# Kernel optimization log

Hardware: AMD Instinct MI355X
Metric: run time of the kernel (lower is better)

Reference implementation:

```python
import jax, jax.numpy as jnp
import numpy as np
from jax import lax

# hyperparameters (match init_kwargs)
N_INP, N_HID, N_OUT = 3, 64, 10
SEQ_LEN, N_ROLL, K = 8, 16, 3
DT, GAMMA, EPS = 0.042, 2.7, 4.7
H, W = 12, 10            # hard-coded in coRNNCell2's PixelwiseConv2d
PAD = (K - 1) // 2
BATCH = 16


def setup_inputs() -> dict:
    key = jax.random.key(0)
    ks = jax.random.split(key, 7)
    x = jax.random.normal(ks[0], (SEQ_LEN, BATCH, N_INP, H, W), dtype=jnp.float32)
    # readin: Conv2d(seq_len*n_inp -> 2*n_hid, k, padding=1, replicate)
    readin_w = jax.random.normal(ks[1], (2 * N_HID, SEQ_LEN * N_INP, K, K), dtype=jnp.float32) * 0.05
    readin_b = jax.random.normal(ks[2], (2 * N_HID,), dtype=jnp.float32) * 0.05
    # PixelwiseConv2d: per-output-pixel weights (out, in, k, k, H, W)
    pw_w = jax.random.normal(ks[3], (N_HID, 2 * N_HID, K, K, H, W), dtype=jnp.float32) * 0.05
    pw_b = jax.random.normal(ks[4], (N_HID, H, W), dtype=jnp.float32) * 0.05
    # readout: 1x1 conv (n_hid -> n_out)
    readout_w = jax.random.normal(ks[5], (N_OUT, N_HID), dtype=jnp.float32) * 0.05
    readout_b = jax.random.normal(ks[6], (N_OUT,), dtype=jnp.float32) * 0.05
    return {"x": x, "readin_w": readin_w, "readin_b": readin_b,
            "pw_w": pw_w, "pw_b": pw_b,
            "readout_w": readout_w, "readout_b": readout_b}


def _pixelwise_conv(x, pw_w, pw_b):
    # x: (B, 2*N_HID, H, W); zero padding like F.unfold(padding=PAD)
    B = x.shape[0]
    xp = jnp.pad(x, ((0, 0), (0, 0), (PAD, PAD), (PAD, PAD)))
    # patches ordered (c, i, j) to match unfold().view(B, C, k, k, H, W)
    patches = jnp.stack([xp[:, :, i:i + H, j:j + W]
                         for i in range(K) for j in range(K)], axis=2)
    patches = patches.reshape(B, 2 * N_HID, K, K, H, W)
    return jnp.einsum('bcijhw,ocijhw->bohw', patches, pw_w) + pw_b[None]


def reference(x, readin_w, readin_b, pw_w, pw_b, readout_w, readout_b):
    T, B = x.shape[0], x.shape[1]
    # 't b c h w -> b (t c) h w'
    xr = jnp.transpose(x, (1, 0, 2, 3, 4)).reshape(B, T * N_INP, H, W)
    # readin conv with replicate padding
    xr_p = jnp.pad(xr, ((0, 0), (0, 0), (PAD, PAD), (PAD, PAD)), mode='edge')
    h = lax.conv_general_dilated(xr_p, readin_w, (1, 1), 'VALID',
                                 dimension_numbers=('NCHW', 'OIHW', 'NCHW'))
    h = h + readin_b[None, :, None, None]
    hy, hz = h[:, :N_HID], h[:, N_HID:]

    def step(carry, _):
        hy, hz = carry
        pre = _pixelwise_conv(jnp.concatenate([hz, hy], axis=1), pw_w, pw_b)
        hz = hz + DT * (jnp.tanh(pre) - GAMMA * hy - EPS * hz)
        hy = hy + DT * hz
        return (hy, hz), None

    (hy, hz), _ = lax.scan(step, (hy, hz), None, length=N_ROLL)
    out = jnp.einsum('bchw,oc->bohw', hy, readout_w) + readout_b[None, :, None, None]
    return out
```

## Files before the change

### kernel.cpp

```cpp
#include <hip/hip_runtime.h>
#include <math.h>

#define N_INPC 3
#define N_HID 64
#define N_OUTC 10
#define SEQ_LEN 8
#define N_ROLL 16
#define DT 0.042f
#define GAMMA 2.7f
#define EPSC 4.7f
#define HH 12
#define WW 10
#define NPIX 120
#define BATCH 16
#define NC 128
#define NK 1152

typedef __attribute__((ext_vector_type(8))) short short8;
typedef __attribute__((ext_vector_type(4))) float f32x4;
typedef unsigned short ushort_t;

__device__ __forceinline__ ushort_t f2bf(float v) {
  union { float f; unsigned u; } x; x.f = v;
  unsigned r = x.u + 0x7fff + ((x.u >> 16) & 1);
  return (ushort_t)(r >> 16);
}

__global__ __launch_bounds__(256) void transpose2_kernel(
    const float* __restrict__ pw_w, ushort_t* __restrict__ Wt) {
  const int t = blockIdx.x * 256 + threadIdx.x;
  if (t >= 120 * 9216) return;
  const int p = t % 120;
  const int rest = t / 120;
  const int o = rest & 15;
  const int kg = (rest >> 4) & 3;
  const int ks = (rest >> 6) % 36;
  const int hot = (rest >> 6) / 36;
  const int o_g = (hot >> 1) * 32 + (hot & 1) * 16 + o;
  const int k0 = ks * 32 + kg * 8;
  ushort_t out8[8];
#pragma unroll
  for (int j = 0; j < 8; ++j) {
    const int kp = k0 + j;
    const int ij = kp >> 7;
    const int c = kp & 127;
    const float v = pw_w[((size_t)o_g * NK + c * 9 + ij) * NPIX + p];
    out8[j] = f2bf(v);
  }
  uint4 pack;
  pack.x = (unsigned)out8[0] | ((unsigned)out8[1] << 16);
  pack.y = (unsigned)out8[2] | ((unsigned)out8[3] << 16);
  pack.z = (unsigned)out8[4] | ((unsigned)out8[5] << 16);
  pack.w = (unsigned)out8[6] | ((unsigned)out8[7] << 16);
  *(uint4*)(Wt + ((size_t)p * 9216 + rest) * 8) = pack;
}

__global__ __launch_bounds__(256) void readin2_kernel(
    const float* __restrict__ x, const float* __restrict__ rw,
    const float* __restrict__ rb, float* __restrict__ Sm,
    ushort_t* __restrict__ Sg) {
  const int n = blockIdx.x * 256 + threadIdx.x;
  if (n >= BATCH * NC * NPIX) return;
  const int p = n % NPIX;
  const int oc = (n / NPIX) & 127;
  const int b = n / (NPIX * NC);
  const int ph = p / WW, pw_ = p % WW;
  float acc = rb[oc];
  for (int ch = 0; ch < SEQ_LEN * N_INPC; ++ch) {
    const int tt = ch / N_INPC, ic = ch % N_INPC;
    const float* xb = x + (((tt * BATCH + b) * N_INPC + ic) * HH) * WW;
    const float* wb = rw + (oc * (SEQ_LEN * N_INPC) + ch) * 9;
#pragma unroll
    for (int di = 0; di < 3; ++di) {
      int ih = ph + di - 1;
      ih = ih < 0 ? 0 : (ih > HH - 1 ? HH - 1 : ih);
#pragma unroll
      for (int dj = 0; dj < 3; ++dj) {
        int iw = pw_ + dj - 1;
        iw = iw < 0 ? 0 : (iw > WW - 1 ? WW - 1 : iw);
        acc += xb[ih * WW + iw] * wb[di * 3 + dj];
      }
    }
  }
  const int sc = (oc < 64) ? (64 + oc) : (oc - 64);
  const size_t idx = ((size_t)(p * BATCH + b)) * NC + sc;
  Sm[idx] = acc;
  Sg[idx] = f2bf(acc);
}

__global__ __launch_bounds__(256) void step2_kernel(
    const ushort_t* __restrict__ Wt, const ushort_t* __restrict__ Sg_cur,
    const float* __restrict__ Sm_cur, ushort_t* __restrict__ Sg_nxt,
    float* __restrict__ Sm_nxt, const float* __restrict__ pwb) {
  __shared__ short8 SA[2304];
  __shared__ f32x4 red[128];
  const int wg = blockIdx.x, p = wg >> 1, h = wg & 1;
  const int ph = p / WW, pw_ = p % WW;
  const int tid = threadIdx.x, wv = tid >> 6, l = tid & 63;

  {
    const int b = tid >> 4, m = tid & 15;
    const int bm = b * NC + m * 8;
#pragma unroll
    for (int q = 0; q < 9; ++q) {
      const int ih = ph + q / 3 - 1, iw = pw_ + q % 3 - 1;
      short8 v = {0, 0, 0, 0, 0, 0, 0, 0};
      if ((unsigned)ih < (unsigned)HH && (unsigned)iw < (unsigned)WW)
        v = *(const short8*)(Sg_cur + (size_t)(ih * WW + iw) * (BATCH * NC) + bm);
      const int row = q * 16 + m;
      SA[row * 16 + (b ^ m)] = v;
    }
  }
  __syncthreads();

  const int ot = wv & 1, kq = wv >> 1;
  const int kg = l >> 4, c16 = l & 15;
  const short8* __restrict__ WB =
      (const short8*)Wt + ((size_t)((p * 2 + h) * 2 + ot)) * 2304 + kg * 16 + c16;
  f32x4 acc0 = {0.f, 0.f, 0.f, 0.f}, acc1 = {0.f, 0.f, 0.f, 0.f};
#pragma unroll
  for (int ii = 0; ii < 9; ++ii) {
    const int ks0 = kq * 18 + ii * 2;
    {
      const int row = ks0 * 4 + kg;
      short8 av = SA[row * 16 + (c16 ^ (row & 15))];
      short8 bv = WB[ks0 * 64];
      acc0 = __builtin_amdgcn_mfma_f32_16x16x32_bf16(av, bv, acc0, 0, 0, 0);
    }
    {
      const int row = (ks0 + 1) * 4 + kg;
      short8 av = SA[row * 16 + (c16 ^ (row & 15))];
      short8 bv = WB[(ks0 + 1) * 64];
      acc1 = __builtin_amdgcn_mfma_f32_16x16x32_bf16(av, bv, acc1, 0, 0, 0);
    }
  }
  f32x4 acc = acc0 + acc1;

  if (wv >= 2) red[(wv - 2) * 64 + l] = acc;
  __syncthreads();
  if (wv < 2) {
    f32x4 part = red[wv * 64 + l];
    acc += part;
    const int o_g = h * 32 + ot * 16 + c16;
    const float pb = pwb[o_g * NPIX + p];
    const int b0 = (l >> 4) * 4;
#pragma unroll
    for (int r = 0; r < 4; ++r) {
      const int b = b0 + r;
      const size_t iz = ((size_t)(p * BATCH + b)) * NC + o_g;
      const float hz = Sm_cur[iz], hy = Sm_cur[iz + 64];
      const float pre = acc[r] + pb;
      const float hzn = hz + DT * (tanhf(pre) - GAMMA * hy - EPSC * hz);
      const float hyn = hy + DT * hzn;
      Sm_nxt[iz] = hzn;
      Sm_nxt[iz + 64] = hyn;
      Sg_nxt[iz] = f2bf(hzn);
      Sg_nxt[iz + 64] = f2bf(hyn);
    }
  }
}

__global__ __launch_bounds__(256) void readout2_kernel(
    const float* __restrict__ Sm, const float* __restrict__ row,
    const float* __restrict__ rob, float* __restrict__ out) {
  const int n = blockIdx.x * 256 + threadIdx.x;
  if (n >= BATCH * N_OUTC * NPIX) return;
  const int p = n % NPIX;
  const int o = (n / NPIX) % N_OUTC;
  const int b = n / (NPIX * N_OUTC);
  float acc = rob[o];
  const float* hy = Sm + ((size_t)(p * BATCH + b)) * NC + 64;
#pragma unroll 8
  for (int c = 0; c < 64; ++c) acc += hy[c] * row[o * 64 + c];
  out[n] = acc;
}

extern "C" void kernel_launch(void* const* d_in, const int* in_sizes, int n_in,
                              void* d_out, int out_size, void* d_ws, size_t ws_size,
                              hipStream_t stream) {
  const float* x         = (const float*)d_in[0];
  const float* readin_w  = (const float*)d_in[1];
  const float* readin_b  = (const float*)d_in[2];
  const float* pw_w      = (const float*)d_in[3];
  const float* pw_b      = (const float*)d_in[4];
  const float* readout_w = (const float*)d_in[5];
  const float* readout_b = (const float*)d_in[6];
  float* out = (float*)d_out;

  ushort_t* Wt  = (ushort_t*)d_ws;
  ushort_t* Sg0 = Wt + (size_t)120 * 9216 * 8;
  ushort_t* Sg1 = Sg0 + 245760;
  float*    Sm0 = (float*)(Sg1 + 245760);
  float*    Sm1 = Sm0 + 245760;

  transpose2_kernel<<<4320, 256, 0, stream>>>(pw_w, Wt);
  readin2_kernel<<<(BATCH * NC * NPIX + 255) / 256, 256, 0, stream>>>(
      x, readin_w, readin_b, Sm0, Sg0);

  ushort_t* gc = Sg0; float* mc = Sm0;
  ushort_t* gn = Sg1; float* mn = Sm1;
  for (int s = 0; s < N_ROLL; ++s) {
    step2_kernel<<<NPIX * 2, 256, 0, stream>>>(Wt, gc, mc, gn, mn, pw_b);
    ushort_t* tg = gc; gc = gn; gn = tg;
    float* tm = mc; mc = mn; mn = tm;
  }
  readout2_kernel<<<(BATCH * N_OUTC * NPIX + 255) / 256, 256, 0, stream>>>(
      mc, readout_w, readout_b, out);
}
```

Before: 212.4 us.

## Fuse recurrent steps into one persistent cooperative kernel with register-resident weights

Replaces the 16 per-step kernel launches with a single cooperative persistent kernel that loops over the time steps and uses grid.sync between them. Each workgroup keeps its bf16 weight slice in registers across all steps, and the fp32 hidden state stays in registers, so only bf16 state is exchanged through global memory. This removes launch gaps and repeated weight and state reloads. In exchange it adds the cost of grid-wide barriers, relies on all 240 blocks being co-resident, and raises register pressure.

Measured after the change: 652.4 us. 3.07x slower.

```diff
diff --git a/kernel.cpp b/kernel.cpp
--- a/kernel.cpp
+++ b/kernel.cpp
@@ -1,5 +1,8 @@
 #include <hip/hip_runtime.h>
+#include <hip/hip_cooperative_groups.h>
 #include <math.h>
+
+namespace cg = cooperative_groups;
 
 #define N_INPC 3
 #define N_HID 64
@@ -44,8 +47,7 @@
     const int kp = k0 + j;
     const int ij = kp >> 7;
     const int c = kp & 127;
-    const float v = pw_w[((size_t)o_g * NK + c * 9 + ij) * NPIX + p];
-    out8[j] = f2bf(v);
+    out8[j] = f2bf(pw_w[((size_t)o_g * NK + c * 9 + ij) * NPIX + p]);
   }
   uint4 pack;
   pack.x = (unsigned)out8[0] | ((unsigned)out8[1] << 16);
@@ -88,74 +90,102 @@
   Sg[idx] = f2bf(acc);
 }
 
-__global__ __launch_bounds__(256) void step2_kernel(
-    const ushort_t* __restrict__ Wt, const ushort_t* __restrict__ Sg_cur,
-    const float* __restrict__ Sm_cur, ushort_t* __restrict__ Sg_nxt,
-    float* __restrict__ Sm_nxt, const float* __restrict__ pwb) {
+__global__ __launch_bounds__(256, 1) void persist_kernel(
+    const ushort_t* __restrict__ Wt, ushort_t* __restrict__ SgA,
+    ushort_t* __restrict__ SgB, float* __restrict__ Sm,
+    const float* __restrict__ pwb) {
+  cg::grid_group grid = cg::this_grid();
   __shared__ short8 SA[2304];
   __shared__ f32x4 red[128];
   const int wg = blockIdx.x, p = wg >> 1, h = wg & 1;
   const int ph = p / WW, pw_ = p % WW;
   const int tid = threadIdx.x, wv = tid >> 6, l = tid & 63;
-
+  const int ot = wv & 1, kq = wv >> 1;
+  const int kg = l >> 4, c16 = l & 15;
+  const int o_g = h * 32 + ot * 16 + c16;
+
+  short8 breg[18];
   {
-    const int b = tid >> 4, m = tid & 15;
-    const int bm = b * NC + m * 8;
+    const short8* __restrict__ WB =
+        (const short8*)Wt + ((size_t)((p * 2 + h) * 2 + ot)) * 2304 + kg * 16 + c16;
+#pragma unroll
+    for (int j = 0; j < 18; ++j) breg[j] = WB[(size_t)(kq * 18 + j) * 64];
+  }
+  const float pb = pwb[o_g * NPIX + p];
+
+  const int b0 = (l >> 4) * 4;
+  float hzr[4], hyr[4];
+  if (wv < 2) {
+#pragma unroll
+    for (int r = 0; r < 4; ++r) {
+      const size_t iz = ((size_t)(p * BATCH + b0 + r)) * NC + o_g;
+      hzr[r] = Sm[iz];
+      hyr[r] = Sm[iz + 64];
+    }
+  }
+
+  const int ab = tid >> 4, am = tid & 15;
+  const int abm = ab * NC + am * 8;
+  ushort_t* sgbuf[2] = {SgA, SgB};
+
+  for (int s = 0; s < N_ROLL; ++s) {
+    const ushort_t* __restrict__ sgc = sgbuf[s & 1];
+    ushort_t* __restrict__ sgn = sgbuf[(s + 1) & 1];
+
 #pragma unroll
     for (int q = 0; q < 9; ++q) {
       const int ih = ph + q / 3 - 1, iw = pw_ + q % 3 - 1;
       short8 v = {0, 0, 0, 0, 0, 0, 0, 0};
       if ((unsigned)ih < (unsigned)HH && (unsigned)iw < (unsigned)WW)
-        v = *(const short8*)(Sg_cur + (size_t)(ih * WW + iw) * (BATCH * NC) + bm);
-      const int row = q * 16 + m;
-      SA[row * 16 + (b ^ m)] = v;
-    }
-  }
-  __syncthreads();
-
-  const int ot = wv & 1, kq = wv >> 1;
-  const int kg = l >> 4, c16 = l & 15;
-  const short8* __restrict__ WB =
-      (const short8*)Wt + ((size_t)((p * 2 + h) * 2 + ot)) * 2304 + kg * 16 + c16;
-  f32x4 acc0 = {0.f, 0.f, 0.f, 0.f}, acc1 = {0.f, 0.f, 0.f, 0.f};
-#pragma unroll
-  for (int ii = 0; ii < 9; ++ii) {
-    const int ks0 = kq * 18 + ii * 2;
-    {
-      const int row = ks0 * 4 + kg;
-      short8 av = SA[row * 16 + (c16 ^ (row & 15))];
-      short8 bv = WB[ks0 * 64];
-      acc0 = __builtin_amdgcn_mfma_f32_16x16x32_bf16(av, bv, acc0, 0, 0, 0);
-    }
-    {
-      const int row = (ks0 + 1) * 4 + kg;
-      short8 av = SA[row * 16 + (c16 ^ (row & 15))];
-      short8 bv = WB[(ks0 + 1) * 64];
-      acc1 = __builtin_amdgcn_mfma_f32_16x16x32_bf16(av, bv, acc1, 0, 0, 0);
-    }
-  }
-  f32x4 acc = acc0 + acc1;
-
-  if (wv >= 2) red[(wv - 2) * 64 + l] = acc;
-  __syncthreads();
+        v = *(const short8*)(sgc + (size_t)(ih * WW + iw) * (BATCH * NC) + abm);
+      const int row = q * 16 + am;
+      SA[row * 16 + (ab ^ am)] = v;
+    }
+    __syncthreads();
+
+    f32x4 acc0 = {0.f, 0.f, 0.f, 0.f}, acc1 = {0.f, 0.f, 0.f, 0.f};
+#pragma unroll
+    for (int ii = 0; ii < 9; ++ii) {
+      const int ks0 = kq * 18 + ii * 2;
+      {
+        const int row = ks0 * 4 + kg;
+        acc0 = __builtin_amdgcn_mfma_f32_16x16x32_bf16(
+            SA[row * 16 + (c16 ^ (row & 15))], breg[ii * 2], acc0, 0, 0, 0);
+      }
+      {
+        const int row = (ks0 + 1) * 4 + kg;
+        acc1 = __builtin_amdgcn_mfma_f32_16x16x32_bf16(
+            SA[row * 16 + (c16 ^ (row & 15))], breg[ii * 2 + 1], acc1, 0, 0, 0);
+      }
+    }
+    f32x4 acc = acc0 + acc1;
+
+    if (wv >= 2) red[(wv - 2) * 64 + l] = acc;
+    __syncthreads();
+    if (wv < 2) {
+      acc += red[wv * 64 + l];
+#pragma unroll
+      for (int r = 0; r < 4; ++r) {
+        const float pre = acc[r] + pb;
+        const float hz = hzr[r], hy = hyr[r];
+        const float hzn = hz + DT * (tanhf(pre) - GAMMA * hy - EPSC * hz);
+        const float hyn = hy + DT * hzn;
+        hzr[r] = hzn;
+        hyr[r] = hyn;
+        const size_t iz = ((size_t)(p * BATCH + b0 + r)) * NC + o_g;
+        sgn[iz] = f2bf(hzn);
+        sgn[iz + 64] = f2bf(hyn);
+      }
+    }
+    grid.sync();
+  }
+
   if (wv < 2) {
-    f32x4 part = red[wv * 64 + l];
-    acc += part;
-    const int o_g = h * 32 + ot * 16 + c16;
-    const float pb = pwb[o_g * NPIX + p];
-    const int b0 = (l >> 4) * 4;
 #pragma unroll
     for (int r = 0; r < 4; ++r) {
-      const int b = b0 + r;
-      const size_t iz = ((size_t)(p * BATCH + b)) * NC + o_g;
-      const float hz = Sm_cur[iz], hy = Sm_cur[iz + 64];
-      const float pre = acc[r] + pb;
-      const float hzn = hz + DT * (tanhf(pre) - GAMMA * hy - EPSC * hz);
-      const float hyn = hy + DT * hzn;
-      Sm_nxt[iz] = hzn;
-      Sm_nxt[iz + 64] = hyn;
-      Sg_nxt[iz] = f2bf(hzn);
-      Sg_nxt[iz + 64] = f2bf(hyn);
+      const size_t iz = ((size_t)(p * BATCH + b0 + r)) * NC + o_g;
+      Sm[iz] = hzr[r];
+      Sm[iz + 64] = hyr[r];
     }
   }
 }
@@ -191,19 +221,23 @@
   ushort_t* Sg0 = Wt + (size_t)120 * 9216 * 8;
   ushort_t* Sg1 = Sg0 + 245760;
   float*    Sm0 = (float*)(Sg1 + 245760);
-  float*    Sm1 = Sm0 + 245760;
 
   transpose2_kernel<<<4320, 256, 0, stream>>>(pw_w, Wt);
   readin2_kernel<<<(BATCH * NC * NPIX + 255) / 256, 256, 0, stream>>>(
       x, readin_w, readin_b, Sm0, Sg0);
 
-  ushort_t* gc = Sg0; float* mc = Sm0;
-  ushort_t* gn = Sg1; float* mn = Sm1;
-  for (int s = 0; s < N_ROLL; ++s) {
-    step2_kernel<<<NPIX * 2, 256, 0, stream>>>(Wt, gc, mc, gn, mn, pw_b);
-    ushort_t* tg = gc; gc = gn; gn = tg;
-    float* tm = mc; mc = mn; mn = tm;
-  }
+  {
+    const ushort_t* aWt = Wt;
+    ushort_t* aSgA = Sg0;
+    ushort_t* aSgB = Sg1;
+    float* aSm = Sm0;
+    const float* aPwb = pw_b;
+    void* args[] = {(void*)&aWt, (void*)&aSgA, (void*)&aSgB,
+                    (void*)&aSm, (void*)&aPwb};
+    hipLaunchCooperativeKernel((const void*)persist_kernel, dim3(NPIX * 2),
+                               dim3(256), args, 0, stream);
+  }
+
   readout2_kernel<<<(BATCH * N_OUTC * NPIX + 255) / 256, 256, 0, stream>>>(
-      mc, readout_w, readout_b, out);
-}
+      Sm0, readout_w, readout_b, out);
+}
```
